# Kernel tuning notes

Hardware: AMD Instinct MI355X
Metric: run time of the kernel (lower is better)

Reference implementation:

```python
import jax, jax.numpy as jnp
import numpy as np

N = 12288      # users + phonePlacements + activities (4096 each)
S = 4096       # per-segment node count
M = 16384      # number of hyperedges
E = 393216     # incidences per branch
F = 256        # in/out channels for both conv layers
C = 128        # model_commonDim
SLOPE = 0.2    # all leaky slopes / negative_slope


def leaky(v, s=SLOPE):
    return jnp.where(v >= 0, v, s * v)


def hconv(h, hyperAttr, ni, ei, W, att, bias, hw):
    """PyG HypergraphConv, use_attention=True, heads=1, dropout=0 (eval)."""
    xl = h @ W                       # [N, F] node features through lin
    ea = hyperAttr @ W               # [M, F] hyperedge attrs through lin
    # attention logits per incidence, grouped-softmax over each node's incidences
    a = jnp.concatenate([xl[ni], ea[ei]], axis=-1) @ att   # [E]
    a = leaky(a, SLOPE)
    amax = jax.ops.segment_max(a, ni, num_segments=N)
    amax = jnp.where(jnp.isfinite(amax), amax, 0.0)
    ae = jnp.exp(a - amax[ni])
    asum = jax.ops.segment_sum(ae, ni, num_segments=N)
    alpha = ae / asum[ni]
    # degree normalizations
    D = jax.ops.segment_sum(hw[ei], ni, num_segments=N)
    Dinv = jnp.where(D > 0, 1.0 / D, 0.0)
    B = jax.ops.segment_sum(jnp.ones((E,), h.dtype), ei, num_segments=M)
    Binv = jnp.where(B > 0, 1.0 / B, 0.0)
    # node -> hyperedge, then hyperedge -> node (alpha applied in both)
    m = jax.ops.segment_sum((Binv[ei] * alpha)[:, None] * xl[ni], ei, num_segments=M)
    out = jax.ops.segment_sum((Dinv[ni] * alpha)[:, None] * m[ei], ni, num_segments=N)
    return out + bias


def setup_inputs() -> dict:
    key = jax.random.key(0)
    ks = jax.random.split(key, 32)
    d = {
        'g': jax.random.normal(ks[0], (N, F), jnp.float32),
        'x': jax.random.normal(ks[1], (4096, F), jnp.float32),
        'hyperWeight': jax.random.uniform(ks[2], (M,), jnp.float32),
        'hyperAttr': jax.random.normal(ks[3], (M, F), jnp.float32),
    }
    for i in range(3):
        d[f'ni{i}'] = jax.random.randint(ks[4 + i], (E,), 0, N).astype(jnp.int32)
        d[f'ei{i}'] = jax.random.randint(ks[7 + i], (E,), 0, M).astype(jnp.int32)
    s = 0.05
    d['W0'] = jax.random.normal(ks[10], (3, F, F), jnp.float32) * s
    d['b0'] = jnp.zeros((3, F), jnp.float32)
    d['Wh1'] = jax.random.normal(ks[11], (3, F, F), jnp.float32) * s
    d['att1'] = jax.random.normal(ks[12], (3, 2 * F), jnp.float32) * s
    d['bc1'] = jnp.zeros((3, F), jnp.float32)
    d['W1'] = jax.random.normal(ks[13], (3, F, F), jnp.float32) * s
    d['b1'] = jnp.zeros((3, F), jnp.float32)
    d['Wh2'] = jax.random.normal(ks[14], (3, F, F), jnp.float32) * s
    d['att2'] = jax.random.normal(ks[15], (3, 2 * F), jnp.float32) * s
    d['bc2'] = jnp.zeros((3, F), jnp.float32)
    d['Wg'] = jax.random.normal(ks[16], (3, F, C), jnp.float32) * s
    d['bg'] = jnp.zeros((3, C), jnp.float32)
    d['Wx'] = jax.random.normal(ks[17], (3, F, C), jnp.float32) * s
    d['bx'] = jnp.zeros((3, C), jnp.float32)
    return d


def reference(g, x, hyperWeight, hyperAttr, ni0, ei0, ni1, ei1, ni2, ei2,
              W0, b0, Wh1, att1, bc1, W1, b1, Wh2, att2, bc2, Wg, bg, Wx, bx):
    nis, eis = (ni0, ni1, ni2), (ei0, ei1, ei2)
    # layer0: per-segment Linear, cat, LeakyReLU
    h = jnp.concatenate([g[i * S:(i + 1) * S] @ W0[i] + b0[i] for i in range(3)], axis=0)
    h = leaky(h)
    # hyper1: 3 conv branches summed, then act1 (dropout=0)
    h = sum(hconv(h, hyperAttr, nis[k], eis[k], Wh1[k], att1[k], bc1[k], hyperWeight)
            for k in range(3))
    h = leaky(h)
    # layer1: per-segment Linear, cat, LeakyReLU
    h = jnp.concatenate([h[i * S:(i + 1) * S] @ W1[i] + b1[i] for i in range(3)], axis=0)
    h = leaky(h)
    # hyper2
    h = sum(hconv(h, hyperAttr, nis[k], eis[k], Wh2[k], att2[k], bc2[k], hyperWeight)
            for k in range(3))
    h = leaky(h)
    # projections to common space
    new_g = [leaky(h[i * S:(i + 1) * S] @ Wg[i] + bg[i]) for i in range(3)]
    xs = [leaky(x @ Wx[i] + bx[i]) for i in range(3)]
    result = jnp.concatenate([xs[1] @ new_g[1].T, xs[2] @ new_g[2].T], axis=1)
    return result, h
```

## Files before the change

kernel.cpp:

```cpp
#include <hip/hip_runtime.h>
#include <cmath>

#define E_INC   393216
#define NN_     12288
#define MM_     16384
#define FDIM    256
#define CDIM    128
#define PKEYS   128
#define LCAP    6144

__host__ __device__ inline int stBase(int r){ return r<3 ? r*(NN_+1) : 3*(NN_+1) + (r-3)*(MM_+1); }
__host__ __device__ inline int nParts(int r){ return (r<3 ? NN_ : MM_) / PKEYS; }

__device__ __forceinline__ float lrelu(float v){ return v >= 0.0f ? v : 0.2f*v; }

struct Ptrs6 { const int* p[6]; };

__global__ __launch_bounds__(256) void coarse_hist(Ptrs6 keys, int* __restrict__ ccnt){
  __shared__ int h[PKEYS];
  int r = blockIdx.y, t = threadIdx.x;
  if (t < PKEYS) h[t] = 0;
  __syncthreads();
  int base = blockIdx.x * 4096;
  const int* ka = keys.p[r];
  for (int j=0;j<16;++j) atomicAdd(&h[ka[base + j*256 + t] >> 7], 1);
  __syncthreads();
  if (t < PKEYS) atomicAdd(&ccnt[r*PKEYS + t], h[t]);
}

__global__ __launch_bounds__(128) void coarse_scan(const int* __restrict__ ccnt,
                                                   int* __restrict__ cstart,
                                                   int* __restrict__ ccur){
  int r = blockIdx.x, t = threadIdx.x;
  int P = nParts(r);
  int c = (t < P) ? ccnt[r*PKEYS + t] : 0;
  __shared__ int sd[128];
  sd[t] = c; __syncthreads();
  for (int ofs=1; ofs<128; ofs<<=1){
    int v = (t>=ofs) ? sd[t-ofs] : 0;
    __syncthreads(); sd[t] += v; __syncthreads();
  }
  int excl = sd[t] - c;
  cstart[r*129 + t] = excl;
  ccur[r*PKEYS + t] = excl;
  if (t == 127) cstart[r*129 + 128] = sd[127];
}

__global__ __launch_bounds__(256) void part_scatter(Ptrs6 keys, int* __restrict__ ccur,
                                                    int* __restrict__ pbuf){
  __shared__ int h[PKEYS];
  __shared__ int cur[PKEYS];
  int r = blockIdx.y, t = threadIdx.x;
  if (t < PKEYS) h[t] = 0;
  __syncthreads();
  int base = blockIdx.x * 4096;
  const int* ka = keys.p[r];
  int myk[16];
  for (int j=0;j<16;++j){
    myk[j] = ka[base + j*256 + t] >> 7;
    atomicAdd(&h[myk[j]], 1);
  }
  __syncthreads();
  if (t < PKEYS) cur[t] = atomicAdd(&ccur[r*PKEYS + t], h[t]);
  __syncthreads();
  int* pb = pbuf + (size_t)r * E_INC;
  for (int j=0;j<16;++j){
    int pos = atomicAdd(&cur[myk[j]], 1);
    pb[pos] = base + j*256 + t;
  }
}

__global__ __launch_bounds__(256) void fine_build(Ptrs6 keys, const int* __restrict__ cstart,
                                                  const int* __restrict__ pbuf,
                                                  int* __restrict__ starts,
                                                  int* __restrict__ lists){
  __shared__ unsigned short kb[LCAP];
  __shared__ int ob[LCAP];
  __shared__ int h[PKEYS], ls[PKEYS], lc[PKEYS];
  int r = blockIdx.y, p = blockIdx.x, t = threadIdx.x;
  int P = nParts(r);
  if (p >= P) return;
  int lo = cstart[r*129 + p], hi = cstart[r*129 + p + 1];
  int len = hi - lo;
  if (t < PKEYS) h[t] = 0;
  __syncthreads();
  const int* ka = keys.p[r];
  const int* pb = pbuf + (size_t)r * E_INC;
  int* lst = lists + (size_t)r * E_INC;
  int kbase = p << 7;
  int sb = stBase(r);
  if (len <= LCAP){
    for (int i=t; i<len; i+=256){
      int e = pb[lo+i];
      int k = ka[e] - kbase;
      kb[i] = (unsigned short)k;
      atomicAdd(&h[k], 1);
    }
    __syncthreads();
    if (t == 0){ int run = 0; for (int k=0;k<PKEYS;++k){ ls[k]=run; lc[k]=run; run+=h[k]; } }
    __syncthreads();
    for (int i=t; i<len; i+=256){
      int pos = atomicAdd(&lc[kb[i]], 1);
      ob[pos] = pb[lo+i];
    }
    __syncthreads();
    for (int i=t; i<len; i+=256) lst[lo+i] = ob[i];
    if (t < PKEYS) starts[sb + kbase + t] = lo + ls[t];
  } else {
    for (int i=t; i<len; i+=256) atomicAdd(&h[ka[pb[lo+i]] - kbase], 1);
    __syncthreads();
    if (t == 0){ int run = 0; for (int k=0;k<PKEYS;++k){ ls[k]=run; lc[k]=run; run+=h[k]; } }
    __syncthreads();
    for (int i=t; i<len; i+=256){
      int e = pb[lo+i];
      int pos = atomicAdd(&lc[ka[e] - kbase], 1);
      lst[lo+pos] = e;
    }
    if (t < PKEYS) starts[sb + kbase + t] = lo + ls[t];
  }
  if (p == P-1 && t == 0) starts[sb + (r<3 ? NN_ : MM_)] = hi;
}

__global__ __launch_bounds__(256) void sortb_kernel(const int* __restrict__ starts,
                                                    int* __restrict__ lists){
  int r = blockIdx.y;
  int nb = (r<3) ? NN_ : MM_;
  int wid = (blockIdx.x*256 + threadIdx.x) >> 6;
  int lane = threadIdx.x & 63;
  if (wid >= nb) return;
  int sb = stBase(r);
  int lo = starts[sb+wid], hi = starts[sb+wid+1];
  int len = hi - lo;
  if (len <= 1) return;
  int* lst = lists + (size_t)r*E_INC;
  if (len <= 64){
    int v = (lane < len) ? lst[lo+lane] : 0x7fffffff;
#pragma unroll
    for (int k = 2; k <= 64; k <<= 1){
#pragma unroll
      for (int j = k>>1; j > 0; j >>= 1){
        int o = __shfl_xor(v, j);
        bool up    = ((lane & k) == 0);
        bool lower = ((lane & j) == 0);
        int mn = min(v,o), mx = max(v,o);
        v = (lower == up) ? mn : mx;
      }
    }
    if (lane < len) lst[lo+lane] = v;
  } else if (lane == 0) {
    for (int i=lo+1; i<hi; ++i){
      int key = lst[i]; int j = i-1;
      while (j>=lo && lst[j]>key){ lst[j+1]=lst[j]; --j; }
      lst[j+1]=key;
    }
  }
}

__global__ __launch_bounds__(256)
void gemm_nn(const float* __restrict__ A, const float* __restrict__ W,
             const float* __restrict__ bias, float* __restrict__ C,
             int N, int segShift, int act)
{
  __shared__ alignas(16) float As[16][132];
  __shared__ alignas(16) float Bs[16][68];
  int t = threadIdx.x;
  int bm = blockIdx.x * 128;
  int bn = blockIdx.y * 64;
  int seg = bm >> segShift;
  const float* Wp = W + (size_t)seg * FDIM * N;
  int tx = t & 15, ty = t >> 4;
  int arow = t >> 1, akq = (t & 1) << 3;
  int brow = t >> 4, bcol = (t & 15) << 2;

  float acc[8][4] = {};
  for (int k0 = 0; k0 < FDIM; k0 += 16){
    const float* ap = A + (size_t)(bm+arow)*FDIM + k0 + akq;
    float4 a0 = *(const float4*)(ap);
    float4 a1 = *(const float4*)(ap + 4);
    As[akq+0][arow]=a0.x; As[akq+1][arow]=a0.y; As[akq+2][arow]=a0.z; As[akq+3][arow]=a0.w;
    As[akq+4][arow]=a1.x; As[akq+5][arow]=a1.y; As[akq+6][arow]=a1.z; As[akq+7][arow]=a1.w;
    *(float4*)&Bs[brow][bcol] = *(const float4*)(Wp + (size_t)(k0+brow)*N + bn + bcol);
    __syncthreads();
#pragma unroll
    for (int kk=0; kk<16; ++kk){
      float4 x0 = *(const float4*)&As[kk][ty<<3];
      float4 x1 = *(const float4*)&As[kk][(ty<<3)+4];
      float4 bv = *(const float4*)&Bs[kk][tx<<2];
      float af[8] = {x0.x,x0.y,x0.z,x0.w,x1.x,x1.y,x1.z,x1.w};
      float bf[4] = {bv.x,bv.y,bv.z,bv.w};
#pragma unroll
      for (int i=0;i<8;++i)
#pragma unroll
        for (int j=0;j<4;++j) acc[i][j] = fmaf(af[i], bf[j], acc[i][j]);
    }
    __syncthreads();
  }
  int c0 = bn + (tx<<2);
  float4 bb = make_float4(0.f,0.f,0.f,0.f);
  if (bias) bb = *(const float4*)(bias + (size_t)seg*N + c0);
#pragma unroll
  for (int i=0;i<8;++i){
    float4 o = make_float4(acc[i][0],acc[i][1],acc[i][2],acc[i][3]);
    if (bias){ o.x+=bb.x; o.y+=bb.y; o.z+=bb.z; o.w+=bb.w; }
    if (act){ o.x=lrelu(o.x); o.y=lrelu(o.y); o.z=lrelu(o.z); o.w=lrelu(o.w); }
    *(float4*)(C + (size_t)(bm+(ty<<3)+i)*N + c0) = o;
  }
}

__global__ __launch_bounds__(256)
void gemm_nt(const float* __restrict__ A, const float* __restrict__ B,
             float* __restrict__ C, int ldc, int colOff)
{
  __shared__ alignas(16) float As[16][132];
  __shared__ alignas(16) float Bs[16][132];
  int t = threadIdx.x;
  int bm = blockIdx.x * 128;
  int bn = blockIdx.y * 128;
  int tx = t & 15, ty = t >> 4;
  int arow = t >> 1, akq = (t & 1) << 3;

  float acc[8][8] = {};
  for (int k0 = 0; k0 < CDIM; k0 += 16){
    const float* ap = A + (size_t)(bm+arow)*CDIM + k0 + akq;
    float4 a0 = *(const float4*)(ap);
    float4 a1 = *(const float4*)(ap + 4);
    As[akq+0][arow]=a0.x; As[akq+1][arow]=a0.y; As[akq+2][arow]=a0.z; As[akq+3][arow]=a0.w;
    As[akq+4][arow]=a1.x; As[akq+5][arow]=a1.y; As[akq+6][arow]=a1.z; As[akq+7][arow]=a1.w;
    const float* bp = B + (size_t)(bn+arow)*CDIM + k0 + akq;
    float4 b0 = *(const float4*)(bp);
    float4 b1 = *(const float4*)(bp + 4);
    Bs[akq+0][arow]=b0.x; Bs[akq+1][arow]=b0.y; Bs[akq+2][arow]=b0.z; Bs[akq+3][arow]=b0.w;
    Bs[akq+4][arow]=b1.x; Bs[akq+5][arow]=b1.y; Bs[akq+6][arow]=b1.z; Bs[akq+7][arow]=b1.w;
    __syncthreads();
#pragma unroll
    for (int kk=0; kk<16; ++kk){
      float4 x0 = *(const float4*)&As[kk][ty<<3];
      float4 x1 = *(const float4*)&As[kk][(ty<<3)+4];
      float4 y0 = *(const float4*)&Bs[kk][tx<<3];
      float4 y1 = *(const float4*)&Bs[kk][(tx<<3)+4];
      float af[8] = {x0.x,x0.y,x0.z,x0.w,x1.x,x1.y,x1.z,x1.w};
      float bf[8] = {y0.x,y0.y,y0.z,y0.w,y1.x,y1.y,y1.z,y1.w};
#pragma unroll
      for (int i=0;i<8;++i)
#pragma unroll
        for (int j=0;j<8;++j) acc[i][j] = fmaf(af[i], bf[j], acc[i][j]);
    }
    __syncthreads();
  }
  int c0 = colOff + bn + (tx<<3);
#pragma unroll
  for (int i=0;i<8;++i){
    float* cp = C + (size_t)(bm+(ty<<3)+i)*ldc + c0;
    *(float4*)(cp)   = make_float4(acc[i][0],acc[i][1],acc[i][2],acc[i][3]);
    *(float4*)(cp+4) = make_float4(acc[i][4],acc[i][5],acc[i][6],acc[i][7]);
  }
}

__global__ __launch_bounds__(256)
void rowdot(const float* __restrict__ Mx, const float* __restrict__ vec,
            float* __restrict__ out, int rows)
{
  int g = blockIdx.x*256 + threadIdx.x;
  int w = g >> 6, lane = g & 63;
  if (w >= rows) return;
  const float* r = Mx + (size_t)w*FDIM;
  double s = 0.0;
#pragma unroll
  for (int c=lane; c<FDIM; c+=64) s = fma((double)r[c], (double)vec[c], s);
  for (int ofs=32; ofs; ofs>>=1) s += __shfl_down(s, ofs);
  if (lane==0) out[w] = (float)s;
}

__global__ __launch_bounds__(256)
void node_stats(const int* __restrict__ starts, const int* __restrict__ list,
                const int* __restrict__ ei, const float* __restrict__ s1,
                const float* __restrict__ s2, const float* __restrict__ hw,
                float* __restrict__ amax, float* __restrict__ asum,
                float* __restrict__ dinv)
{
  int g = blockIdx.x*256 + threadIdx.x;
  int w = g >> 6, lane = g & 63;
  if (w >= NN_) return;
  int lo = starts[w], hi = starts[w+1];
  float s1n = s1[w];
  float mx = -INFINITY;
  for (int i=lo+lane; i<hi; i+=64){
    int e = list[i];
    mx = fmaxf(mx, lrelu(s1n + s2[ei[e]]));
  }
  for (int ofs=32; ofs; ofs>>=1) mx = fmaxf(mx, __shfl_xor(mx, ofs));
  if (lo == hi) mx = 0.0f;
  double se = 0.0, sd = 0.0;
  for (int i=lo+lane; i<hi; i+=64){
    int e = list[i]; int m = ei[e];
    float a = lrelu(s1n + s2[m]);
    se += (double)expf(a - mx);
    sd += (double)hw[m];
  }
  for (int ofs=32; ofs; ofs>>=1){ se += __shfl_xor(se, ofs); sd += __shfl_xor(sd, ofs); }
  if (lane==0){
    amax[w] = mx;
    asum[w] = (float)se;
    float D = (float)sd;
    dinv[w] = (D > 0.0f) ? 1.0f/D : 0.0f;
  }
}

__global__ __launch_bounds__(256)
void alpha_kernel(const int* __restrict__ ni, const int* __restrict__ ei,
                  const float* __restrict__ s1, const float* __restrict__ s2,
                  const float* __restrict__ amax, const float* __restrict__ asum,
                  float* __restrict__ alpha)
{
  int e = blockIdx.x*256 + threadIdx.x;
  int n = ni[e];
  float a = lrelu(s1[n] + s2[ei[e]]);
  alpha[e] = expf(a - amax[n]) / asum[n];
}

__global__ __launch_bounds__(256)
void m_kernel(const int* __restrict__ estarts, const int* __restrict__ elist,
              const int* __restrict__ ni, const float* __restrict__ alpha,
              const float* __restrict__ xl, float* __restrict__ m)
{
  int g = blockIdx.x*256 + threadIdx.x;
  int w = g >> 6, lane = g & 63;
  if (w >= MM_) return;
  int lo = estarts[w], hi = estarts[w+1];
  float binv = (hi > lo) ? 1.0f/(float)(hi-lo) : 0.0f;
  float ax=0.f, ay=0.f, az=0.f, aw=0.f;
  int col = lane << 2;
  for (int i=lo; i<hi; ++i){
    int e = elist[i];
    float c = __fmul_rn(binv, alpha[e]);
    const float4 x4 = *(const float4*)(xl + (size_t)ni[e]*FDIM + col);
    ax = __fadd_rn(ax, __fmul_rn(c, x4.x));
    ay = __fadd_rn(ay, __fmul_rn(c, x4.y));
    az = __fadd_rn(az, __fmul_rn(c, x4.z));
    aw = __fadd_rn(aw, __fmul_rn(c, x4.w));
  }
  *(float4*)(m + (size_t)w*FDIM + col) = make_float4(ax,ay,az,aw);
}

__global__ __launch_bounds__(256)
void out_kernel(const int* __restrict__ nstarts, const int* __restrict__ nlist,
                const int* __restrict__ ei, const float* __restrict__ alpha,
                const float* __restrict__ dinv, const float* __restrict__ m,
                const float* __restrict__ bias, float* __restrict__ accb,
                int first, int finalAct)
{
  int g = blockIdx.x*256 + threadIdx.x;
  int w = g >> 6, lane = g & 63;
  if (w >= NN_) return;
  int lo = nstarts[w], hi = nstarts[w+1];
  float dv = dinv[w];
  float ax=0.f, ay=0.f, az=0.f, aw=0.f;
  int col = lane << 2;
  for (int i=lo; i<hi; ++i){
    int e = nlist[i];
    float c = __fmul_rn(dv, alpha[e]);
    const float4 m4 = *(const float4*)(m + (size_t)ei[e]*FDIM + col);
    ax = __fadd_rn(ax, __fmul_rn(c, m4.x));
    ay = __fadd_rn(ay, __fmul_rn(c, m4.y));
    az = __fadd_rn(az, __fmul_rn(c, m4.z));
    aw = __fadd_rn(aw, __fmul_rn(c, m4.w));
  }
  const float4 b4 = *(const float4*)(bias + col);
  ax = __fadd_rn(ax, b4.x); ay = __fadd_rn(ay, b4.y);
  az = __fadd_rn(az, b4.z); aw = __fadd_rn(aw, b4.w);
  float* p = accb + (size_t)w*FDIM + col;
  if (!first){
    float4 pr = *(const float4*)p;
    ax = __fadd_rn(pr.x, ax); ay = __fadd_rn(pr.y, ay);
    az = __fadd_rn(pr.z, az); aw = __fadd_rn(pr.w, aw);
  }
  if (finalAct){ ax=lrelu(ax); ay=lrelu(ay); az=lrelu(az); aw=lrelu(aw); }
  *(float4*)p = make_float4(ax,ay,az,aw);
}

extern "C" void kernel_launch(void* const* d_in, const int* in_sizes, int n_in,
                              void* d_out, int out_size, void* d_ws, size_t ws_size,
                              hipStream_t stream)
{
  (void)in_sizes; (void)n_in; (void)out_size; (void)ws_size;
  const float* g     = (const float*)d_in[0];
  const float* x     = (const float*)d_in[1];
  const float* hw    = (const float*)d_in[2];
  const float* hattr = (const float*)d_in[3];
  const int* ni[3]   = {(const int*)d_in[4], (const int*)d_in[6], (const int*)d_in[8]};
  const int* ei[3]   = {(const int*)d_in[5], (const int*)d_in[7], (const int*)d_in[9]};
  const float* W0  = (const float*)d_in[10];
  const float* b0  = (const float*)d_in[11];
  const float* Wh1 = (const float*)d_in[12];
  const float* att1= (const float*)d_in[13];
  const float* bc1 = (const float*)d_in[14];
  const float* W1  = (const float*)d_in[15];
  const float* b1  = (const float*)d_in[16];
  const float* Wh2 = (const float*)d_in[17];
  const float* att2= (const float*)d_in[18];
  const float* bc2 = (const float*)d_in[19];
  const float* Wg  = (const float*)d_in[20];
  const float* bg  = (const float*)d_in[21];
  const float* Wx  = (const float*)d_in[22];
  const float* bx  = (const float*)d_in[23];
  float* outp = (float*)d_out;

  char* base = (char*)d_ws;
  size_t off = 0;
  auto alloc = [&](size_t bytes)->void*{
    void* p = base + off;
    off = (off + bytes + 255) & ~(size_t)255;
    return p;
  };
  const size_t SZ_H = (size_t)NN_*FDIM;
  float* hA    = (float*)alloc(SZ_H*4);
  float* xl    = (float*)alloc(SZ_H*4);
  float* acc   = (float*)alloc(SZ_H*4);
  float* mbuf  = (float*)alloc((size_t)MM_*FDIM*4);
  float* alphab= (float*)alloc((size_t)E_INC*4);
  float* s1    = (float*)alloc(NN_*4);
  float* s2    = (float*)alloc(MM_*4);
  float* vv    = (float*)alloc(FDIM*4);
  float* amax  = (float*)alloc(NN_*4);
  float* asum  = (float*)alloc(NN_*4);
  float* dinvb = (float*)alloc(NN_*4);
  float* ng1   = (float*)alloc((size_t)4096*CDIM*4);
  float* ng2   = (float*)alloc((size_t)4096*CDIM*4);
  float* xs1   = (float*)alloc((size_t)4096*CDIM*4);
  float* xs2   = (float*)alloc((size_t)4096*CDIM*4);
  int*   ccnt  = (int*)alloc((size_t)6*PKEYS*4);
  int*   ccur  = (int*)alloc((size_t)6*PKEYS*4);
  int*   cstart= (int*)alloc((size_t)6*129*4);
  int*   stb   = (int*)alloc((size_t)(3*(NN_+1)+3*(MM_+1))*4);
  int*   lists = (int*)alloc((size_t)6*E_INC*4);
  int*   pbuf  = (int*)mbuf;

  hipMemsetAsync(ccnt, 0, (size_t)6*PKEYS*4, stream);
  Ptrs6 ip{{ni[0],ni[1],ni[2],ei[0],ei[1],ei[2]}};
  coarse_hist <<<dim3(96,6),256,0,stream>>>(ip, ccnt);
  coarse_scan <<<6,128,0,stream>>>(ccnt, cstart, ccur);
  part_scatter<<<dim3(96,6),256,0,stream>>>(ip, ccur, pbuf);
  fine_build  <<<dim3(128,6),256,0,stream>>>(ip, cstart, pbuf, stb, lists);
  sortb_kernel<<<dim3(4096,6),256,0,stream>>>(stb, lists);

  gemm_nn<<<dim3(96,4),256,0,stream>>>(g, W0, b0, hA, FDIM, 12, 1);

  auto hyper = [&](const float* hin, const float* Whs, const float* atts, const float* bcs){
    for (int k=0;k<3;++k){
      const float* Wk   = Whs + (size_t)k*FDIM*FDIM;
      const float* attA = atts + (size_t)k*2*FDIM;
      const float* attB = attA + FDIM;
      const int* nst = stb + stBase(k);
      const int* nls = lists + (size_t)k*E_INC;
      const int* est = stb + stBase(3+k);
      const int* els = lists + (size_t)(3+k)*E_INC;
      gemm_nn    <<<dim3(96,4),256,0,stream>>>(hin, Wk, nullptr, xl, FDIM, 30, 0);
      rowdot     <<<64,  256,0,stream>>>(Wk, attB, vv, FDIM);
      rowdot     <<<3072,256,0,stream>>>(xl, attA, s1, NN_);
      rowdot     <<<4096,256,0,stream>>>(hattr, vv, s2, MM_);
      node_stats <<<3072,256,0,stream>>>(nst, nls, ei[k], s1, s2, hw, amax, asum, dinvb);
      alpha_kernel<<<E_INC/256,256,0,stream>>>(ni[k], ei[k], s1, s2, amax, asum, alphab);
      m_kernel   <<<4096,256,0,stream>>>(est, els, ni[k], alphab, xl, mbuf);
      out_kernel <<<3072,256,0,stream>>>(nst, nls, ei[k], alphab, dinvb, mbuf,
                                         bcs + (size_t)k*FDIM, acc, k==0, k==2);
    }
  };

  hyper(hA, Wh1, att1, bc1);
  gemm_nn<<<dim3(96,4),256,0,stream>>>(acc, W1, b1, hA, FDIM, 12, 1);
  hyper(hA, Wh2, att2, bc2);

  gemm_nn<<<dim3(32,2),256,0,stream>>>(acc + (size_t)1*4096*FDIM, Wg + (size_t)1*FDIM*CDIM,
                                       bg + 1*CDIM, ng1, CDIM, 30, 1);
  gemm_nn<<<dim3(32,2),256,0,stream>>>(acc + (size_t)2*4096*FDIM, Wg + (size_t)2*FDIM*CDIM,
                                       bg + 2*CDIM, ng2, CDIM, 30, 1);
  gemm_nn<<<dim3(32,2),256,0,stream>>>(x, Wx + (size_t)1*FDIM*CDIM, bx + 1*CDIM, xs1, CDIM, 30, 1);
  gemm_nn<<<dim3(32,2),256,0,stream>>>(x, Wx + (size_t)2*FDIM*CDIM, bx + 2*CDIM, xs2, CDIM, 30, 1);

  gemm_nt<<<dim3(32,32),256,0,stream>>>(xs1, ng1, outp, 8192, 0);
  gemm_nt<<<dim3(32,32),256,0,stream>>>(xs2, ng2, outp, 8192, 4096);

  hipMemcpyAsync(outp + (size_t)4096*8192, acc, SZ_H*4, hipMemcpyDeviceToDevice, stream);
}
```

Measured before the change: 1.829 ms.

## Fuse attention stats and alpha, batch s2 precompute, unroll gathers, drop final copy

Moves the hyperedge attention logits for all six conv configurations into one upfront pass. The per-node s1 dot product, softmax stats and alpha computation are fused into a single per-node kernel, which removes the separate rowdot and alpha launches and the amax/asum buffers. The m and out gather loops are unrolled to issue 8 row loads before accumulating, for more memory-level parallelism. The last out_kernel also writes h straight into the output, replacing the trailing device copy, and the two Wg projection GEMMs merge into one launch. The cost is more register pressure in the unrolled loops and a second store stream in the final out_kernel.

```diff
diff --git a/kernel.cpp b/kernel.cpp
--- a/kernel.cpp
+++ b/kernel.cpp
@@ -257,32 +257,70 @@
 }
 
 __global__ __launch_bounds__(256)
-void rowdot(const float* __restrict__ Mx, const float* __restrict__ vec,
-            float* __restrict__ out, int rows)
+void vv_all(const float* __restrict__ Wh1, const float* __restrict__ Wh2,
+            const float* __restrict__ att1, const float* __restrict__ att2,
+            float* __restrict__ vvb)
 {
   int g = blockIdx.x*256 + threadIdx.x;
   int w = g >> 6, lane = g & 63;
-  if (w >= rows) return;
-  const float* r = Mx + (size_t)w*FDIM;
+  if (w >= 6*FDIM) return;
+  int cfg = w >> 8, rr = w & 255;
+  int l = cfg / 3, k = cfg % 3;
+  const float* r = (l ? Wh2 : Wh1) + (size_t)k*FDIM*FDIM + (size_t)rr*FDIM;
+  const float* vec = (l ? att2 : att1) + (size_t)k*2*FDIM + FDIM;
   double s = 0.0;
 #pragma unroll
   for (int c=lane; c<FDIM; c+=64) s = fma((double)r[c], (double)vec[c], s);
   for (int ofs=32; ofs; ofs>>=1) s += __shfl_down(s, ofs);
-  if (lane==0) out[w] = (float)s;
-}
-
-__global__ __launch_bounds__(256)
-void node_stats(const int* __restrict__ starts, const int* __restrict__ list,
-                const int* __restrict__ ei, const float* __restrict__ s1,
-                const float* __restrict__ s2, const float* __restrict__ hw,
-                float* __restrict__ amax, float* __restrict__ asum,
-                float* __restrict__ dinv)
+  if (lane==0) vvb[cfg*FDIM + rr] = (float)s;
+}
+
+__global__ __launch_bounds__(256)
+void s2_all(const float* __restrict__ hattr, const float* __restrict__ vvb,
+            float* __restrict__ s2all)
+{
+  __shared__ float vs[6*FDIM];
+  int t = threadIdx.x;
+  for (int i=t; i<6*FDIM; i+=256) vs[i] = vvb[i];
+  __syncthreads();
+  int g = blockIdx.x*256 + t;
+  int w = g >> 6, lane = g & 63;
+  if (w >= MM_) return;
+  const float* r = hattr + (size_t)w*FDIM;
+  double s[6] = {0,0,0,0,0,0};
+#pragma unroll
+  for (int c=lane; c<FDIM; c+=64){
+    double xv = (double)r[c];
+#pragma unroll
+    for (int q=0;q<6;++q) s[q] = fma(xv, (double)vs[q*FDIM + c], s[q]);
+  }
+#pragma unroll
+  for (int q=0;q<6;++q){
+    double v = s[q];
+    for (int ofs=32; ofs; ofs>>=1) v += __shfl_down(v, ofs);
+    if (lane==0) s2all[(size_t)q*MM_ + w] = (float)v;
+  }
+}
+
+__global__ __launch_bounds__(256)
+void node_alpha(const int* __restrict__ starts, const int* __restrict__ list,
+                const int* __restrict__ ei, const float* __restrict__ xl,
+                const float* __restrict__ attA, const float* __restrict__ s2,
+                const float* __restrict__ hw,
+                float* __restrict__ dinv, float* __restrict__ alpha)
 {
   int g = blockIdx.x*256 + threadIdx.x;
   int w = g >> 6, lane = g & 63;
   if (w >= NN_) return;
+  const float* r = xl + (size_t)w*FDIM;
+  double s = 0.0;
+#pragma unroll
+  for (int c=lane; c<FDIM; c+=64) s = fma((double)r[c], (double)attA[c], s);
+  for (int ofs=32; ofs; ofs>>=1) s += __shfl_down(s, ofs);
+  s = __shfl(s, 0);
+  float s1n = (float)s;
+
   int lo = starts[w], hi = starts[w+1];
-  float s1n = s1[w];
   float mx = -INFINITY;
   for (int i=lo+lane; i<hi; i+=64){
     int e = list[i];
@@ -298,24 +336,16 @@
     sd += (double)hw[m];
   }
   for (int ofs=32; ofs; ofs>>=1){ se += __shfl_xor(se, ofs); sd += __shfl_xor(sd, ofs); }
+  float sumf = (float)se;
   if (lane==0){
-    amax[w] = mx;
-    asum[w] = (float)se;
     float D = (float)sd;
     dinv[w] = (D > 0.0f) ? 1.0f/D : 0.0f;
   }
-}
-
-__global__ __launch_bounds__(256)
-void alpha_kernel(const int* __restrict__ ni, const int* __restrict__ ei,
-                  const float* __restrict__ s1, const float* __restrict__ s2,
-                  const float* __restrict__ amax, const float* __restrict__ asum,
-                  float* __restrict__ alpha)
-{
-  int e = blockIdx.x*256 + threadIdx.x;
-  int n = ni[e];
-  float a = lrelu(s1[n] + s2[ei[e]]);
-  alpha[e] = expf(a - amax[n]) / asum[n];
+  for (int i=lo+lane; i<hi; i+=64){
+    int e = list[i];
+    float a = lrelu(s1n + s2[ei[e]]);
+    alpha[e] = expf(a - mx) / sumf;
+  }
 }
 
 __global__ __launch_bounds__(256)
@@ -330,14 +360,24 @@
   float binv = (hi > lo) ? 1.0f/(float)(hi-lo) : 0.0f;
   float ax=0.f, ay=0.f, az=0.f, aw=0.f;
   int col = lane << 2;
-  for (int i=lo; i<hi; ++i){
-    int e = elist[i];
-    float c = __fmul_rn(binv, alpha[e]);
-    const float4 x4 = *(const float4*)(xl + (size_t)ni[e]*FDIM + col);
-    ax = __fadd_rn(ax, __fmul_rn(c, x4.x));
-    ay = __fadd_rn(ay, __fmul_rn(c, x4.y));
-    az = __fadd_rn(az, __fmul_rn(c, x4.z));
-    aw = __fadd_rn(aw, __fmul_rn(c, x4.w));
+  int i = lo;
+  while (i < hi){
+    int nc = hi - i; if (nc > 8) nc = 8;
+    float4 v[8]; float c[8];
+#pragma unroll
+    for (int j=0;j<8;++j) if (j < nc){
+      int e = elist[i+j];
+      c[j] = __fmul_rn(binv, alpha[e]);
+      v[j] = *(const float4*)(xl + (size_t)ni[e]*FDIM + col);
+    }
+#pragma unroll
+    for (int j=0;j<8;++j) if (j < nc){
+      ax = __fadd_rn(ax, __fmul_rn(c[j], v[j].x));
+      ay = __fadd_rn(ay, __fmul_rn(c[j], v[j].y));
+      az = __fadd_rn(az, __fmul_rn(c[j], v[j].z));
+      aw = __fadd_rn(aw, __fmul_rn(c[j], v[j].w));
+    }
+    i += nc;
   }
   *(float4*)(m + (size_t)w*FDIM + col) = make_float4(ax,ay,az,aw);
 }
@@ -347,7 +387,7 @@
                 const int* __restrict__ ei, const float* __restrict__ alpha,
                 const float* __restrict__ dinv, const float* __restrict__ m,
                 const float* __restrict__ bias, float* __restrict__ accb,
-                int first, int finalAct)
+                float* __restrict__ mirror, int first, int finalAct)
 {
   int g = blockIdx.x*256 + threadIdx.x;
   int w = g >> 6, lane = g & 63;
@@ -356,14 +396,24 @@
   float dv = dinv[w];
   float ax=0.f, ay=0.f, az=0.f, aw=0.f;
   int col = lane << 2;
-  for (int i=lo; i<hi; ++i){
-    int e = nlist[i];
-    float c = __fmul_rn(dv, alpha[e]);
-    const float4 m4 = *(const float4*)(m + (size_t)ei[e]*FDIM + col);
-    ax = __fadd_rn(ax, __fmul_rn(c, m4.x));
-    ay = __fadd_rn(ay, __fmul_rn(c, m4.y));
-    az = __fadd_rn(az, __fmul_rn(c, m4.z));
-    aw = __fadd_rn(aw, __fmul_rn(c, m4.w));
+  int i = lo;
+  while (i < hi){
+    int nc = hi - i; if (nc > 8) nc = 8;
+    float4 v[8]; float c[8];
+#pragma unroll
+    for (int j=0;j<8;++j) if (j < nc){
+      int e = nlist[i+j];
+      c[j] = __fmul_rn(dv, alpha[e]);
+      v[j] = *(const float4*)(m + (size_t)ei[e]*FDIM + col);
+    }
+#pragma unroll
+    for (int j=0;j<8;++j) if (j < nc){
+      ax = __fadd_rn(ax, __fmul_rn(c[j], v[j].x));
+      ay = __fadd_rn(ay, __fmul_rn(c[j], v[j].y));
+      az = __fadd_rn(az, __fmul_rn(c[j], v[j].z));
+      aw = __fadd_rn(aw, __fmul_rn(c[j], v[j].w));
+    }
+    i += nc;
   }
   const float4 b4 = *(const float4*)(bias + col);
   ax = __fadd_rn(ax, b4.x); ay = __fadd_rn(ay, b4.y);
@@ -375,7 +425,9 @@
     az = __fadd_rn(pr.z, az); aw = __fadd_rn(pr.w, aw);
   }
   if (finalAct){ ax=lrelu(ax); ay=lrelu(ay); az=lrelu(az); aw=lrelu(aw); }
-  *(float4*)p = make_float4(ax,ay,az,aw);
+  float4 o = make_float4(ax,ay,az,aw);
+  *(float4*)p = o;
+  if (mirror) *(float4*)(mirror + (size_t)w*FDIM + col) = o;
 }
 
 extern "C" void kernel_launch(void* const* d_in, const int* in_sizes, int n_in,
@@ -418,14 +470,10 @@
   float* acc   = (float*)alloc(SZ_H*4);
   float* mbuf  = (float*)alloc((size_t)MM_*FDIM*4);
   float* alphab= (float*)alloc((size_t)E_INC*4);
-  float* s1    = (float*)alloc(NN_*4);
-  float* s2    = (float*)alloc(MM_*4);
-  float* vv    = (float*)alloc(FDIM*4);
-  float* amax  = (float*)alloc(NN_*4);
-  float* asum  = (float*)alloc(NN_*4);
+  float* vvb   = (float*)alloc((size_t)6*FDIM*4);
+  float* s2all = (float*)alloc((size_t)6*MM_*4);
   float* dinvb = (float*)alloc(NN_*4);
-  float* ng1   = (float*)alloc((size_t)4096*CDIM*4);
-  float* ng2   = (float*)alloc((size_t)4096*CDIM*4);
+  float* ngbuf = (float*)alloc((size_t)8192*CDIM*4);
   float* xs1   = (float*)alloc((size_t)4096*CDIM*4);
   float* xs2   = (float*)alloc((size_t)4096*CDIM*4);
   int*   ccnt  = (int*)alloc((size_t)6*PKEYS*4);
@@ -443,42 +491,39 @@
   fine_build  <<<dim3(128,6),256,0,stream>>>(ip, cstart, pbuf, stb, lists);
   sortb_kernel<<<dim3(4096,6),256,0,stream>>>(stb, lists);
 
+  vv_all<<<384,256,0,stream>>>(Wh1, Wh2, att1, att2, vvb);
+  s2_all<<<4096,256,0,stream>>>(hattr, vvb, s2all);
+
   gemm_nn<<<dim3(96,4),256,0,stream>>>(g, W0, b0, hA, FDIM, 12, 1);
 
-  auto hyper = [&](const float* hin, const float* Whs, const float* atts, const float* bcs){
+  auto hyper = [&](int layer, const float* hin, const float* Whs, const float* atts,
+                   const float* bcs, float* mirror){
     for (int k=0;k<3;++k){
       const float* Wk   = Whs + (size_t)k*FDIM*FDIM;
       const float* attA = atts + (size_t)k*2*FDIM;
-      const float* attB = attA + FDIM;
+      const float* s2   = s2all + (size_t)(layer*3+k)*MM_;
       const int* nst = stb + stBase(k);
       const int* nls = lists + (size_t)k*E_INC;
       const int* est = stb + stBase(3+k);
       const int* els = lists + (size_t)(3+k)*E_INC;
-      gemm_nn    <<<dim3(96,4),256,0,stream>>>(hin, Wk, nullptr, xl, FDIM, 30, 0);
-      rowdot     <<<64,  256,0,stream>>>(Wk, attB, vv, FDIM);
-      rowdot     <<<3072,256,0,stream>>>(xl, attA, s1, NN_);
-      rowdot     <<<4096,256,0,stream>>>(hattr, vv, s2, MM_);
-      node_stats <<<3072,256,0,stream>>>(nst, nls, ei[k], s1, s2, hw, amax, asum, dinvb);
-      alpha_kernel<<<E_INC/256,256,0,stream>>>(ni[k], ei[k], s1, s2, amax, asum, alphab);
-      m_kernel   <<<4096,256,0,stream>>>(est, els, ni[k], alphab, xl, mbuf);
-      out_kernel <<<3072,256,0,stream>>>(nst, nls, ei[k], alphab, dinvb, mbuf,
-                                         bcs + (size_t)k*FDIM, acc, k==0, k==2);
+      gemm_nn   <<<dim3(96,4),256,0,stream>>>(hin, Wk, nullptr, xl, FDIM, 30, 0);
+      node_alpha<<<3072,256,0,stream>>>(nst, nls, ei[k], xl, attA, s2, hw, dinvb, alphab);
+      m_kernel  <<<4096,256,0,stream>>>(est, els, ni[k], alphab, xl, mbuf);
+      out_kernel<<<3072,256,0,stream>>>(nst, nls, ei[k], alphab, dinvb, mbuf,
+                                        bcs + (size_t)k*FDIM, acc,
+                                        (k==2) ? mirror : nullptr, k==0, k==2);
     }
   };
 
-  hyper(hA, Wh1, att1, bc1);
+  hyper(0, hA, Wh1, att1, bc1, nullptr);
   gemm_nn<<<dim3(96,4),256,0,stream>>>(acc, W1, b1, hA, FDIM, 12, 1);
-  hyper(hA, Wh2, att2, bc2);
-
-  gemm_nn<<<dim3(32,2),256,0,stream>>>(acc + (size_t)1*4096*FDIM, Wg + (size_t)1*FDIM*CDIM,
-                                       bg + 1*CDIM, ng1, CDIM, 30, 1);
-  gemm_nn<<<dim3(32,2),256,0,stream>>>(acc + (size_t)2*4096*FDIM, Wg + (size_t)2*FDIM*CDIM,
-                                       bg + 2*CDIM, ng2, CDIM, 30, 1);
+  hyper(1, hA, Wh2, att2, bc2, outp + (size_t)4096*8192);
+
+  gemm_nn<<<dim3(64,2),256,0,stream>>>(acc + (size_t)4096*FDIM, Wg + (size_t)FDIM*CDIM,
+                                       bg + CDIM, ngbuf, CDIM, 12, 1);
   gemm_nn<<<dim3(32,2),256,0,stream>>>(x, Wx + (size_t)1*FDIM*CDIM, bx + 1*CDIM, xs1, CDIM, 30, 1);
   gemm_nn<<<dim3(32,2),256,0,stream>>>(x, Wx + (size_t)2*FDIM*CDIM, bx + 2*CDIM, xs2, CDIM, 30, 1);
 
-  gemm_nt<<<dim3(32,32),256,0,stream>>>(xs1, ng1, outp, 8192, 0);
-  gemm_nt<<<dim3(32,32),256,0,stream>>>(xs2, ng2, outp, 8192, 4096);
-
-  hipMemcpyAsync(outp + (size_t)4096*8192, acc, SZ_H*4, hipMemcpyDeviceToDevice, stream);
-}
+  gemm_nt<<<dim3(32,32),256,0,stream>>>(xs1, ngbuf, outp, 8192, 0);
+  gemm_nt<<<dim3(32,32),256,0,stream>>>(xs2, ngbuf + (size_t)4096*CDIM, outp, 8192, 4096);
+}
```

New measurement: 1.659 ms. -9.3%, faster.
